# Kernel optimization log

Measured on AMD Instinct MI355X. Metric: run time of the kernel, lower is better.

Reference implementation:

```python
import jax, jax.numpy as jnp
import numpy as np
from jax.scipy.linalg import solve_triangular

B, S, H, D, L = 8, 256, 768, 128, 64


def setup_inputs() -> dict:
    key = jax.random.key(0)
    ks = jax.random.split(key, 14)
    f = lambda k, shp, s=1.0: (jax.random.normal(k, shp, dtype=jnp.float32) * s)
    return {
        'word_feat_mean': f(ks[0], (B, S, H)),
        'word_feat_div': f(ks[1], (B, S, H)),
        'sent_feat_mean': f(ks[2], (B, 1, H)),
        'sent_feat_div': f(ks[3], (B, 1, H)),
        'W1': f(ks[4], (H, D), 0.02), 'b1': f(ks[5], (D,), 0.02),
        'W2': f(ks[6], (H, D), 0.02), 'b2': f(ks[7], (D,), 0.02),
        'W3': f(ks[8], (H, D), 0.02), 'b3': f(ks[9], (D,), 0.02),
        'W4': f(ks[10], (H, D), 0.02), 'b4': f(ks[11], (D,), 0.02),
        'label_mean': f(ks[12], (L, D)),
        'label_div_vec': f(ks[13], (L, D)),
    }


def _jsd_rank1(mu_p, v_p, mu_q, v_q):
    """Symmetric Gaussian JSD (0.5*(KL12+KL21)) between N(mu_p, I+v_p v_p^T) (labels, [L,D])
    and N(mu_q, I+v_q v_q^T) (words, [B,S,D]) via Sherman-Morrison closed form -> [B,L,S].
    Same math as torch.distributions MVN KL with Sigma = I + vv^T."""
    d = mu_p.shape[-1]
    n_p = 1.0 + jnp.sum(v_p * v_p, -1)            # [L]   = det(I+vp vp^T)
    n_q = 1.0 + jnp.sum(v_q * v_q, -1)            # [B,S]
    dot = jnp.einsum('ld,bsd->bls', v_p, v_q)     # vp.vq
    # ||mu_q - mu_p||^2 expanded without materializing [B,L,S,D]
    d2 = (jnp.sum(mu_q * mu_q, -1)[:, None, :]
          - 2.0 * jnp.einsum('ld,bsd->bls', mu_p, mu_q)
          + jnp.sum(mu_p * mu_p, -1)[None, :, None])
    vq_delta = (jnp.einsum('bsd,bsd->bs', v_q, mu_q)[:, None, :]
                - jnp.einsum('ld,bsd->bls', mu_p, v_q))
    vp_delta = (jnp.einsum('ld,bsd->bls', v_p, mu_q)
                - jnp.sum(v_p * mu_p, -1)[None, :, None])
    n_p_b = n_p[None, :, None]
    n_q_b = n_q[:, None, :]
    maha_q = d2 - vq_delta ** 2 / n_q_b           # delta^T Sigma_q^{-1} delta
    maha_p = d2 - vp_delta ** 2 / n_p_b
    tr_pq = d + (n_p_b - 1.0) - ((n_q_b - 1.0) + dot ** 2) / n_q_b  # tr(Sq^{-1} Sp)
    tr_qp = d + (n_q_b - 1.0) - ((n_p_b - 1.0) + dot ** 2) / n_p_b
    kl_pq = 0.5 * (jnp.log(n_q_b) - jnp.log(n_p_b) - d + tr_pq + maha_q)
    kl_qp = 0.5 * (jnp.log(n_p_b) - jnp.log(n_q_b) - d + tr_qp + maha_p)
    return 0.5 * (kl_pq + kl_qp)


def _jsd_full(mu_p, S_p, mu_q, S_q):
    """Symmetric JSD between full-covariance Gaussians, Cholesky-based (like torch MVN KL).
    mu_*: [..., D], S_*: [..., D, D] -> [...]."""
    d = mu_p.shape[-1]
    L_p = jnp.linalg.cholesky(S_p)
    L_q = jnp.linalg.cholesky(S_q)
    logdet_p = 2.0 * jnp.sum(jnp.log(jnp.diagonal(L_p, axis1=-2, axis2=-1)), -1)
    logdet_q = 2.0 * jnp.sum(jnp.log(jnp.diagonal(L_q, axis1=-2, axis2=-1)), -1)
    delta = mu_q - mu_p

    def kl(La, Lb, logda, logdb):
        # KL(a||b) = 0.5*(logdet_b - logdet_a - d + tr(Sb^{-1}Sa) + delta^T Sb^{-1} delta)
        X = solve_triangular(Lb, La, lower=True)
        tr = jnp.sum(X * X, axis=(-1, -2))
        y = solve_triangular(Lb, delta[..., None], lower=True)[..., 0]
        maha = jnp.sum(y * y, -1)
        return 0.5 * (logdb - logda - d + tr + maha)

    return 0.5 * (kl(L_p, L_q, logdet_p, logdet_q) + kl(L_q, L_p, logdet_q, logdet_p))


def reference(word_feat_mean, word_feat_div, sent_feat_mean, sent_feat_div,
              W1, b1, W2, b2, W3, b3, W4, b4, label_mean, label_div_vec):
    Bx, Sx, _ = word_feat_mean.shape
    Dx = W1.shape[1]
    Lx = label_mean.shape[0]
    wm = word_feat_mean @ W1 + b1        # jw1: [B,S,D]
    wv = word_feat_div @ W2 + b2         # jw2: [B,S,D]
    sm = sent_feat_mean @ W3 + b3        # jw3: [B,1,D]
    sv = sent_feat_div @ W4 + b4         # jw4: [B,1,D]
    eye = jnp.eye(Dx, dtype=wm.dtype)
    # Gaussian JSD attention: q = labels, k = v = words (closed-form, no [B,L*S,D,D])
    score = jax.nn.softmax(_jsd_rank1(label_mean, label_div_vec, wm, wv), axis=-1)  # [B,L,S]
    v_mean = jnp.einsum('bls,bsd->bld', score, wm)
    word_cov = eye + wv[..., :, None] * wv[..., None, :]                 # [B,S,D,D]
    v_div = jnp.einsum('bls,bsde->blde', score, word_cov)                # [B,L,D,D]
    sent_cov = eye + sv[..., :, None] * sv[..., None, :]                 # [B,1,D,D]
    text_mean = (sm + v_mean) / 2                                        # [B,L,D]
    text_div = (sent_cov + v_div) / 2                                    # [B,L,D,D]
    label_cov = eye + label_div_vec[:, :, None] * label_div_vec[:, None, :]  # [L,D,D]
    lm_b = jnp.broadcast_to(label_mean, (Bx, Lx, Dx))
    lc_b = jnp.broadcast_to(label_cov, (Bx, Lx, Dx, Dx))
    relate_score = _jsd_full(text_mean, text_div, lm_b, lc_b)            # [B,L]
    return relate_score, lm_b, lc_b
```

## Files before the change

### kernel.cpp

```cpp
#include <hip/hip_runtime.h>
#include <hip/hip_bf16.h>


#define PITCH 132

typedef __attribute__((ext_vector_type(8))) short bf16x8;
typedef __attribute__((ext_vector_type(4))) float f32x4;

__device__ __forceinline__ float bf2f(unsigned int u) {
    union { unsigned int i; float f; } c; c.i = u << 16; return c.f;
}
__device__ __forceinline__ unsigned short f2bf(float f) {
    __hip_bfloat16 h = __float2bfloat16(f);
    union { __hip_bfloat16 h; unsigned short u; } c; c.h = h; return c.u;
}

__global__ __launch_bounds__(256, 2)
void k1_gemm(const float* __restrict__ Am, const float* __restrict__ Av,
             const float* __restrict__ sfm, const float* __restrict__ sfd,
             const float* __restrict__ W1, const float* __restrict__ B1,
             const float* __restrict__ W2, const float* __restrict__ B2,
             const float* __restrict__ W3, const float* __restrict__ B3,
             const float* __restrict__ W4, const float* __restrict__ B4,
             const float* __restrict__ lm, const float* __restrict__ ldv,
             float* __restrict__ wm, float* __restrict__ wv,
             float* __restrict__ sm, float* __restrict__ sv,
             float4* __restrict__ labscg,
             unsigned short* __restrict__ wvTg) {
    const int tid = threadIdx.x;
    const int sel = blockIdx.y;
    if (blockIdx.x == 257) {
        if (sel == 0) {
            int l = tid >> 2, q = tid & 3;
            const float* mr = lm + (size_t)l * 128 + q * 32;
            const float* vr = ldv + (size_t)l * 128 + q * 32;
            float s0 = 0.f, s1 = 0.f, s2 = 0.f;
            for (int k = 0; k < 32; k += 4) {
                float4 m = *(const float4*)&mr[k];
                float4 v = *(const float4*)&vr[k];
                s0 += m.x * m.x + m.y * m.y + m.z * m.z + m.w * m.w;
                s1 += v.x * v.x + v.y * v.y + v.z * v.z + v.w * v.w;
                s2 += m.x * v.x + m.y * v.y + m.z * v.z + m.w * v.w;
            }
            s0 += __shfl_xor(s0, 1); s0 += __shfl_xor(s0, 2);
            s1 += __shfl_xor(s1, 1); s1 += __shfl_xor(s1, 2);
            s2 += __shfl_xor(s2, 1); s2 += __shfl_xor(s2, 2);
            if (q == 0) labscg[l] = make_float4(s0, s1, s2, 0.f);
        }
        return;
    }
    __shared__ float At[8][64];
    __shared__ __align__(16) float Wt[64][128];
    __shared__ float tileT[8][129];
    const bool sentB = (blockIdx.x == 256);
    const float* A  = sentB ? (sel ? sfd : sfm) : (sel ? Av : Am);
    const float* W  = sentB ? (sel ? W4 : W3) : (sel ? W2 : W1);
    const float* Bs = sentB ? (sel ? B4 : B3) : (sel ? B2 : B1);
    float* D = sentB ? (sel ? sv : sm) : (sel ? wv : wm);
    const int R0 = sentB ? 0 : blockIdx.x * 8;
    const int r = tid >> 5;
    const int j0 = (tid & 31) * 4;
    float acc[4] = {0.f, 0.f, 0.f, 0.f};
    for (int k0 = 0; k0 < 768; k0 += 64) {
        __syncthreads();
        {
            int f = tid;
            At[f >> 6][f & 63] = A[(size_t)(R0 + (f >> 6)) * 768 + k0 + (f & 63)];
            f = tid + 256;
            At[f >> 6][f & 63] = A[(size_t)(R0 + (f >> 6)) * 768 + k0 + (f & 63)];
        }
#pragma unroll
        for (int it = 0; it < 8; ++it) {
            int f = tid + it * 256;
            int rr = f >> 5, c4 = (f & 31) * 4;
            *(float4*)&Wt[rr][c4] = *(const float4*)&W[(size_t)(k0 + rr) * 128 + c4];
        }
        __syncthreads();
#pragma unroll 16
        for (int kk = 0; kk < 64; ++kk) {
            float a = At[r][kk];
            float4 w0 = *(const float4*)&Wt[kk][j0];
            acc[0] += a * w0.x; acc[1] += a * w0.y; acc[2] += a * w0.z; acc[3] += a * w0.w;
        }
    }
    {
        float b0 = Bs[j0], b1 = Bs[j0 + 1], b2 = Bs[j0 + 2], b3 = Bs[j0 + 3];
        float4 o = make_float4(acc[0] + b0, acc[1] + b1, acc[2] + b2, acc[3] + b3);
        *(float4*)&D[(size_t)(R0 + r) * 128 + j0] = o;
        tileT[r][j0 + 0] = o.x; tileT[r][j0 + 1] = o.y;
        tileT[r][j0 + 2] = o.z; tileT[r][j0 + 3] = o.w;
    }
    if (sel && !sentB) {
        __syncthreads();
        if (tid < 128) {
            int d = tid;
            unsigned short u[8];
#pragma unroll
            for (int ss = 0; ss < 8; ++ss) u[ss] = f2bf(tileT[ss][d]);
            unsigned int p0 = (unsigned int)u[0] | ((unsigned int)u[1] << 16);
            unsigned int p1 = (unsigned int)u[2] | ((unsigned int)u[3] << 16);
            unsigned int p2 = (unsigned int)u[4] | ((unsigned int)u[5] << 16);
            unsigned int p3 = (unsigned int)u[6] | ((unsigned int)u[7] << 16);
            unsigned short* dst = wvTg + (size_t)(R0 >> 8) * 32768 + (size_t)d * 256 + (R0 & 255);
            *(uint4*)dst = make_uint4(p0, p1, p2, p3);
        }
    }
}

template <int N>
__device__ __forceinline__ void bsumN(float* v, float* red) {
#pragma unroll
    for (int o = 32; o; o >>= 1)
#pragma unroll
        for (int n = 0; n < N; ++n) v[n] += __shfl_xor(v[n], o);
    __syncthreads();
    if ((threadIdx.x & 63) == 0) {
        int w = threadIdx.x >> 6;
#pragma unroll
        for (int n = 0; n < N; ++n) red[w * N + n] = v[n];
    }
    __syncthreads();
#pragma unroll
    for (int n = 0; n < N; ++n)
        v[n] = red[0 * N + n] + red[1 * N + n] + red[2 * N + n] + red[3 * N + n];
    __syncthreads();
}

__global__ __launch_bounds__(256, 2)
void k4_fused(const float* __restrict__ wm, const float* __restrict__ wv,
              const unsigned short* __restrict__ wvTg,
              const float* __restrict__ smg, const float* __restrict__ svg,
              const float* __restrict__ lmg, const float* __restrict__ ldvg,
              const float4* __restrict__ labscg,
              float* __restrict__ out) {
    extern __shared__ float smem[];
    float* Amat = smem;
    float* Wb   = smem + 16896;
    float* ssq  = smem + 19008;
    float* svr  = smem + 19264;
    float* vrow = smem + 19392;
    float* zv   = smem + 19520;
    float* zd   = smem + 19648;
    float* red  = smem + 19776;
    float* scoreL = Amat;
    float* vpart  = Amat + 256;

    const int tid = threadIdx.x;
    const int bid = blockIdx.x;
    const int b = bid >> 6, l = bid & 63;

    if (tid < 128) {
        svr[tid]  = svg[b * 128 + tid];
        vrow[tid] = ldvg[l * 128 + tid];
        zv[tid]   = lmg[l * 128 + tid];
    }
    __syncthreads();
    if (tid < 32) {
        float4 v = *(const float4*)&lmg[l * 128 + tid * 4];
        *(float4*)&out[512 + (size_t)bid * 128 + tid * 4] = v;
    }
    {
        float* lcb = out + 512 + 65536 + (size_t)bid * 16384;
#pragma unroll
        for (int q = 0; q < 16; ++q) {
            int flat4 = q * 256 + tid;
            int i = flat4 >> 5;
            int j4 = (flat4 & 31) * 4;
            float vi = vrow[i];
            float4 r;
            r.x = vi * vrow[j4 + 0] + ((i == j4 + 0) ? 1.f : 0.f);
            r.y = vi * vrow[j4 + 1] + ((i == j4 + 1) ? 1.f : 0.f);
            r.z = vi * vrow[j4 + 2] + ((i == j4 + 2) ? 1.f : 0.f);
            r.w = vi * vrow[j4 + 3] + ((i == j4 + 3) ? 1.f : 0.f);
            *(float4*)&lcb[(size_t)flat4 * 4] = r;
        }
    }
    float4 lsv = labscg[l];
    const float mmp = lsv.x, np = 1.f + lsv.y, vmp = lsv.z;
    const float4* wmr = (const float4*)(wm + (size_t)(b * 256 + tid) * 128);
    const float4* wvr = (const float4*)(wv + (size_t)(b * 256 + tid) * 128);
    float md = 0.f, dot = 0.f, pvv = 0.f, vq = 0.f;
    float smm = 0.f, svv = 0.f, smv = 0.f;
#pragma unroll 8
    for (int q = 0; q < 32; ++q) {
        float4 xm = wmr[q], xv = wvr[q];
        const float* m4 = &zv[q * 4];
        const float* v4 = &vrow[q * 4];
        md  += m4[0] * xm.x + m4[1] * xm.y + m4[2] * xm.z + m4[3] * xm.w;
        dot += v4[0] * xv.x + v4[1] * xv.y + v4[2] * xv.z + v4[3] * xv.w;
        pvv += m4[0] * xv.x + m4[1] * xv.y + m4[2] * xv.z + m4[3] * xv.w;
        vq  += v4[0] * xm.x + v4[1] * xm.y + v4[2] * xm.z + v4[3] * xm.w;
        smm += xm.x * xm.x + xm.y * xm.y + xm.z * xm.z + xm.w * xm.w;
        svv += xv.x * xv.x + xv.y * xv.y + xv.z * xv.z + xv.w * xv.w;
        smv += xm.x * xv.x + xm.y * xv.y + xm.z * xv.z + xm.w * xv.w;
    }
    float nq = 1.f + svv;
    float d2 = smm - 2.f * md + mmp;
    float vqd = smv - pvv, vpd = vq - vmp;
    float inq = 1.f / nq, inp = 1.f / np;
    float maha_q = d2 - vqd * vqd * inq;
    float maha_p = d2 - vpd * vpd * inp;
    float logit = 0.25f * ((np - 1.f) + (nq - 1.f)
                           - (nq - 1.f + dot * dot) * inq
                           - (np - 1.f + dot * dot) * inp
                           + maha_q + maha_p);
    float mx = logit;
#pragma unroll
    for (int o = 32; o; o >>= 1) mx = fmaxf(mx, __shfl_xor(mx, o));
    if ((tid & 63) == 0) red[tid >> 6] = mx;
    __syncthreads();
    mx = fmaxf(fmaxf(red[0], red[1]), fmaxf(red[2], red[3]));
    float e = expf(logit - mx);
    float s = e;
#pragma unroll
    for (int o = 32; o; o >>= 1) s += __shfl_xor(s, o);
    __syncthreads();
    if ((tid & 63) == 0) red[tid >> 6] = s;
    __syncthreads();
    float tot = red[0] + red[1] + red[2] + red[3];
    float sc = e / tot;
    scoreL[tid] = sc;
    ssq[tid] = sqrtf(sc);
    __syncthreads();
    {
        int d4 = (tid & 31) * 4, sg = tid >> 5;
        const float* wmb = wm + (size_t)b * 256 * 128;
        float ax = 0.f, ay = 0.f, az = 0.f, aw = 0.f;
        for (int s2 = sg * 32; s2 < sg * 32 + 32; ++s2) {
            float w = scoreL[s2];
            float4 x = *(const float4*)&wmb[(size_t)s2 * 128 + d4];
            ax += w * x.x; ay += w * x.y; az += w * x.z; aw += w * x.w;
        }
        *(float4*)&vpart[sg * 128 + d4] = make_float4(ax, ay, az, aw);
    }
    __syncthreads();
    if (tid < 128) {
        float vm8 = 0.f;
#pragma unroll
        for (int g2 = 0; g2 < 8; ++g2) vm8 += vpart[g2 * 128 + tid];
        zd[tid] = zv[tid] - 0.5f * (smg[b * 128 + tid] + vm8);
        zv[tid] = vrow[tid];
    }
    __syncthreads();
    {
        unsigned short* Sb = (unsigned short*)Amat;
        const unsigned short* src = wvTg + (size_t)b * 32768;
        const int s0 = (tid & 31) * 8;
        float ssv[8];
#pragma unroll
        for (int j = 0; j < 8; ++j) ssv[j] = ssq[s0 + j];
#pragma unroll
        for (int it = 0; it < 16; ++it) {
            int f8 = tid + it * 256;
            int d = f8 >> 5;
            uint4 raw = *(const uint4*)&src[(size_t)f8 * 8];
            unsigned int p0 = (unsigned int)f2bf(bf2f(raw.x & 0xffffu) * ssv[0])
                            | ((unsigned int)f2bf(bf2f(raw.x >> 16) * ssv[1]) << 16);
            unsigned int p1 = (unsigned int)f2bf(bf2f(raw.y & 0xffffu) * ssv[2])
                            | ((unsigned int)f2bf(bf2f(raw.y >> 16) * ssv[3]) << 16);
            unsigned int p2 = (unsigned int)f2bf(bf2f(raw.z & 0xffffu) * ssv[4])
                            | ((unsigned int)f2bf(bf2f(raw.z >> 16) * ssv[5]) << 16);
            unsigned int p3 = (unsigned int)f2bf(bf2f(raw.w & 0xffffu) * ssv[6])
                            | ((unsigned int)f2bf(bf2f(raw.w >> 16) * ssv[7]) << 16);
            *(uint4*)&Sb[(size_t)d * 264 + s0] = make_uint4(p0, p1, p2, p3);
        }
    }
    __syncthreads();
    {
        const unsigned short* Sb = (const unsigned short*)Amat;
        const int w = tid >> 6, ln = tid & 63;
        const int rl = ln & 15, g = ln >> 4;
        const int arow0 = 16 * w + rl;
        const int arow1 = 16 * (w + 4) + rl;
        f32x4 acc0[8], acc1[8];
#pragma unroll
        for (int t = 0; t < 8; ++t) {
            acc0[t] = (f32x4){0.f, 0.f, 0.f, 0.f};
            acc1[t] = (f32x4){0.f, 0.f, 0.f, 0.f};
        }
#pragma unroll
        for (int ks = 0; ks < 8; ++ks) {
            bf16x8 a0 = *(const bf16x8*)&Sb[(size_t)arow0 * 264 + ks * 32 + g * 8];
            bf16x8 a1 = *(const bf16x8*)&Sb[(size_t)arow1 * 264 + ks * 32 + g * 8];
#pragma unroll
            for (int tj = 0; tj < 8; ++tj) {
                bf16x8 bb = *(const bf16x8*)&Sb[(size_t)(16 * tj + rl) * 264 + ks * 32 + g * 8];
                acc0[tj] = __builtin_amdgcn_mfma_f32_16x16x32_bf16(a0, bb, acc0[tj], 0, 0, 0);
                acc1[tj] = __builtin_amdgcn_mfma_f32_16x16x32_bf16(a1, bb, acc1[tj], 0, 0, 0);
            }
        }
        __syncthreads();
#pragma unroll
        for (int tj = 0; tj < 8; ++tj) {
            int j = 16 * tj + rl;
            float svj = svr[j];
#pragma unroll
            for (int r = 0; r < 4; ++r) {
                int i = 16 * w + g * 4 + r;
                Amat[i * PITCH + j] = ((i == j) ? 1.f : 0.f) + 0.5f * (svr[i] * svj + acc0[tj][r]);
                int i2 = 16 * (w + 4) + g * 4 + r;
                Amat[i2 * PITCH + j] = ((i2 == j) ? 1.f : 0.f) + 0.5f * (svr[i2] * svj + acc1[tj][r]);
            }
        }
    }
    __syncthreads();
    float v5[5] = {0.f, 0.f, 0.f, 0.f, 0.f};
    if (tid < 128) {
        v5[0] = Amat[tid * PITCH + tid];
        float vv = vrow[tid], de = zd[tid];
        v5[1] = vv * vv; v5[2] = de * de; v5[3] = vv * de;
    }
    {
        int i = tid >> 1, h = tid & 1;
        const float* Ar = &Amat[i * PITCH + h * 64];
        const float* vr = &vrow[h * 64];
        float s2 = 0.f;
        for (int k2 = 0; k2 < 64; k2 += 4) {
            float4 a = *(const float4*)&Ar[k2];
            s2 += a.x * vr[k2] + a.y * vr[k2 + 1] + a.z * vr[k2 + 2] + a.w * vr[k2 + 3];
        }
        v5[4] = vrow[i] * s2;
    }
    bsumN<5>(v5, red);
    const float trP = v5[0], nv = v5[1], dds = v5[2], vds = v5[3], vsv = v5[4];
    for (int p = 0; p < 8; ++p) {
        const int base = 16 * p;
        const int R = 112 - base;
        __syncthreads();
        if (p > 0) {
            const int pb = base - 16;
            if (tid >= base && tid < 128) {
                int i = tid;
                const float* Lr = &Amat[i * PITCH + pb];
                float dv = 0.f, dd2 = 0.f;
#pragma unroll
                for (int t = 0; t < 16; ++t) {
                    float lvv = Lr[t];
                    dv  += lvv * zv[pb + t];
                    dd2 += lvv * zd[pb + t];
                }
                zv[i] -= dv; zd[i] -= dd2;
            }
            int njobs = (R + 16) * 16;
            for (int idx = tid; idx < njobs; idx += 256) {
                int r2 = idx >> 4, jc = idx & 15;
                int i = base + r2, j = base + jc;
                if (j <= i) {
                    const float* wi = &Wb[i];
                    const float* wj = &Wb[j];
                    float acc2 = 0.f;
#pragma unroll
                    for (int t2 = 0; t2 < 16; ++t2)
                        acc2 += wi[t2 * PITCH] * wj[t2 * PITCH];
                    Amat[i * PITCH + j] -= acc2;
                }
            }
        }
        __syncthreads();
        if (tid < 64) {
            const int c = tid;
            float cv[16];
            if (c < 16) {
#pragma unroll
                for (int r2 = 0; r2 < 16; ++r2) {
                    int hi = (r2 >= c) ? r2 : c, lo2 = (r2 >= c) ? c : r2;
                    cv[r2] = Amat[(base + hi) * PITCH + base + lo2];
                }
            } else {
#pragma unroll
                for (int r2 = 0; r2 < 16; ++r2) cv[r2] = 0.f;
            }
#pragma unroll
            for (int t = 0; t < 16; ++t) {
                float lt[16];
#pragma unroll
                for (int r2 = 0; r2 < 16; ++r2) lt[r2] = __shfl(cv[r2], t);
                float invs = 1.f / sqrtf(lt[t]);
                if (c == t) {
#pragma unroll
                    for (int r2 = 0; r2 < 16; ++r2) cv[r2] = (r2 >= t) ? lt[r2] * invs : 0.f;
                } else if (c > t && c < 16) {
                    float lc = lt[c] * invs;
#pragma unroll
                    for (int r2 = 0; r2 < 16; ++r2)
                        if (r2 > t) cv[r2] -= (lt[r2] * invs) * lc;
                }
            }
            float x[16], acb[16];
#pragma unroll
            for (int r2 = 0; r2 < 16; ++r2) acb[r2] = 0.f;
#pragma unroll
            for (int r2 = 0; r2 < 16; ++r2) {
                float Lrr = __shfl(cv[r2], r2);
                float xr = (((c == r2) ? 1.f : 0.f) - acb[r2]) / Lrr;
                x[r2] = xr;
#pragma unroll
                for (int q = r2 + 1; q < 16; ++q) acb[q] += __shfl(cv[q], r2) * xr;
            }
            if (c < 16) {
#pragma unroll
                for (int r2 = 0; r2 < 16; ++r2)
                    Amat[(base + c) * PITCH + base + r2] = x[r2];
            }
            if (c < 32) {
                int t2 = c & 15;
                float* zp = (c < 16) ? zv : zd;
                float a0 = 0.f;
#pragma unroll
                for (int a = 0; a < 16; ++a)
                    a0 += Amat[(base + a) * PITCH + base + t2] * zp[base + a];
                zp[base + t2] = a0;
            }
        } else if (p > 0 && R > 0) {
            int nt = R >> 3;
            int ntri = (nt * (nt + 1)) >> 1;
            for (int tau = tid - 64; tau < ntri; tau += 192) {
                float ft = sqrtf(8.f * (float)tau + 1.f);
                int tr = (int)((ft - 1.f) * 0.5f);
                while (((tr + 1) * (tr + 2)) / 2 <= tau) ++tr;
                while ((tr * (tr + 1)) / 2 > tau) --tr;
                int tc = tau - ((tr * (tr + 1)) >> 1);
                int ii = base + 16 + tr * 8, jj = base + 16 + tc * 8;
                float a2[8][8];
#pragma unroll
                for (int r2 = 0; r2 < 8; ++r2)
#pragma unroll
                    for (int c2 = 0; c2 < 8; ++c2) a2[r2][c2] = 0.f;
#pragma unroll
                for (int t = 0; t < 16; ++t) {
                    const float* wr = &Wb[t * PITCH];
                    float4 x0 = *(const float4*)&wr[ii];
                    float4 x1 = *(const float4*)&wr[ii + 4];
                    float4 y0 = *(const float4*)&wr[jj];
                    float4 y1 = *(const float4*)&wr[jj + 4];
                    float xa[8] = {x0.x,x0.y,x0.z,x0.w, x1.x,x1.y,x1.z,x1.w};
                    float yb[8] = {y0.x,y0.y,y0.z,y0.w, y1.x,y1.y,y1.z,y1.w};
#pragma unroll
                    for (int r2 = 0; r2 < 8; ++r2)
#pragma unroll
                        for (int c2 = 0; c2 < 8; ++c2) a2[r2][c2] += xa[r2] * yb[c2];
                }
#pragma unroll
                for (int r2 = 0; r2 < 8; ++r2) {
                    float* Ar2 = &Amat[(ii + r2) * PITCH + jj];
                    float4 u0 = *(float4*)&Ar2[0];
                    float4 u1 = *(float4*)&Ar2[4];
                    u0.x -= a2[r2][0]; u0.y -= a2[r2][1]; u0.z -= a2[r2][2]; u0.w -= a2[r2][3];
                    u1.x -= a2[r2][4]; u1.y -= a2[r2][5]; u1.z -= a2[r2][6]; u1.w -= a2[r2][7];
                    *(float4*)&Ar2[0] = u0;
                    *(float4*)&Ar2[4] = u1;
                }
            }
        }
        __syncthreads();
        if (R > 0 && tid < R) {
            int i = base + 16 + tid;
            const float* Ar = &Amat[i * PITCH + base];
            float4 q0 = *(const float4*)&Ar[0];
            float4 q1 = *(const float4*)&Ar[4];
            float4 q2 = *(const float4*)&Ar[8];
            float4 q3 = *(const float4*)&Ar[12];
            float rA[16] = {q0.x,q0.y,q0.z,q0.w, q1.x,q1.y,q1.z,q1.w,
                            q2.x,q2.y,q2.z,q2.w, q3.x,q3.y,q3.z,q3.w};
            float lo[16];
#pragma unroll
            for (int t = 0; t < 16; ++t) lo[t] = 0.f;
#pragma unroll
            for (int a = 0; a < 16; ++a) {
                float va = rA[a];
                const float* Trow = &Amat[(base + a) * PITCH + base];
                float4 t0 = *(const float4*)&Trow[0];
                float4 t1 = *(const float4*)&Trow[4];
                float4 t2 = *(const float4*)&Trow[8];
                float4 t3 = *(const float4*)&Trow[12];
                lo[0] += va * t0.x; lo[1] += va * t0.y; lo[2] += va * t0.z; lo[3] += va * t0.w;
                lo[4] += va * t1.x; lo[5] += va * t1.y; lo[6] += va * t1.z; lo[7] += va * t1.w;
                lo[8] += va * t2.x; lo[9] += va * t2.y; lo[10] += va * t2.z; lo[11] += va * t2.w;
                lo[12] += va * t3.x; lo[13] += va * t3.y; lo[14] += va * t3.z; lo[15] += va * t3.w;
            }
            float* Aw = &Amat[i * PITCH + base];
            *(float4*)&Aw[0]  = make_float4(lo[0], lo[1], lo[2], lo[3]);
            *(float4*)&Aw[4]  = make_float4(lo[4], lo[5], lo[6], lo[7]);
            *(float4*)&Aw[8]  = make_float4(lo[8], lo[9], lo[10], lo[11]);
            *(float4*)&Aw[12] = make_float4(lo[12], lo[13], lo[14], lo[15]);
#pragma unroll
            for (int t = 0; t < 16; ++t) Wb[t * PITCH + i] = lo[t];
        }
    }
    __syncthreads();
    for (int t = tid; t < 128; t += 256) {
        int q = t >> 5, tt = t & 31;
        int c0 = (tt >> 2) * 2, r0 = (tt & 3) * 4;
        int rb = 32 * q + 16, cb = 32 * q;
        float a4[2][4] = {{0,0,0,0},{0,0,0,0}};
        for (int k = 0; k < 16; k += 4) {
            float4 xc0 = *(const float4*)&Amat[(cb + c0) * PITCH + cb + k];
            float4 xc1 = *(const float4*)&Amat[(cb + c0 + 1) * PITCH + cb + k];
#pragma unroll
            for (int rr = 0; rr < 4; ++rr) {
                float4 lr = *(const float4*)&Amat[(rb + r0 + rr) * PITCH + cb + k];
                a4[0][rr] += xc0.x * lr.x + xc0.y * lr.y + xc0.z * lr.z + xc0.w * lr.w;
                a4[1][rr] += xc1.x * lr.x + xc1.y * lr.y + xc1.z * lr.z + xc1.w * lr.w;
            }
        }
#pragma unroll
        for (int cc = 0; cc < 2; ++cc)
#pragma unroll
            for (int rr = 0; rr < 4; ++rr)
                Wb[q * 256 + (c0 + cc) * 16 + (r0 + rr)] = a4[cc][rr];
    }
    __syncthreads();
    for (int t = tid; t < 128; t += 256) {
        int q = t >> 5, tt = t & 31;
        int c0 = (tt >> 2) * 2, r0 = (tt & 3) * 4;
        int rb = 32 * q + 16, cb = 32 * q;
        float a4[2][4] = {{0,0,0,0},{0,0,0,0}};
        for (int a = 0; a < 16; ++a) {
            float y0 = Wb[q * 256 + c0 * 16 + a];
            float y1 = Wb[q * 256 + (c0 + 1) * 16 + a];
            float4 t2 = *(const float4*)&Amat[(rb + a) * PITCH + rb + r0];
            a4[0][0] += y0 * t2.x; a4[0][1] += y0 * t2.y; a4[0][2] += y0 * t2.z; a4[0][3] += y0 * t2.w;
            a4[1][0] += y1 * t2.x; a4[1][1] += y1 * t2.y; a4[1][2] += y1 * t2.z; a4[1][3] += y1 * t2.w;
        }
#pragma unroll
        for (int cc = 0; cc < 2; ++cc)
#pragma unroll
            for (int rr = 0; rr < 4; ++rr)
                Amat[(cb + c0 + cc) * PITCH + rb + r0 + rr] = -a4[cc][rr];
    }
    __syncthreads();
    {
        int q = tid >> 7, tt = tid & 127;
        int c0 = (tt >> 3) * 2, r0 = (tt & 7) * 4;
        int rb = 64 * q + 32, cb = 64 * q;
        int ks = c0 & ~15;
        float a4[2][4] = {{0,0,0,0},{0,0,0,0}};
        for (int k = ks; k < 32; k += 4) {
            float4 xc0 = *(const float4*)&Amat[(cb + c0) * PITCH + cb + k];
            float4 xc1 = *(const float4*)&Amat[(cb + c0 + 1) * PITCH + cb + k];
#pragma unroll
            for (int rr = 0; rr < 4; ++rr) {
                float4 lr = *(const float4*)&Amat[(rb + r0 + rr) * PITCH + cb + k];
                a4[0][rr] += xc0.x * lr.x + xc0.y * lr.y + xc0.z * lr.z + xc0.w * lr.w;
                a4[1][rr] += xc1.x * lr.x + xc1.y * lr.y + xc1.z * lr.z + xc1.w * lr.w;
            }
        }
#pragma unroll
        for (int cc = 0; cc < 2; ++cc)
#pragma unroll
            for (int rr = 0; rr < 4; ++rr)
                Wb[q * 1024 + (c0 + cc) * 32 + (r0 + rr)] = a4[cc][rr];
    }
    __syncthreads();
    {
        int q = tid >> 7, tt = tid & 127;
        int c0 = (tt >> 3) * 2, r0 = (tt & 7) * 4;
        int rb = 64 * q + 32, cb = 64 * q;
        int atop = (r0 & ~15) + 15;
        float a4[2][4] = {{0,0,0,0},{0,0,0,0}};
        for (int a = 0; a <= atop; ++a) {
            float y0 = Wb[q * 1024 + c0 * 32 + a];
            float y1 = Wb[q * 1024 + (c0 + 1) * 32 + a];
            float4 t2 = *(const float4*)&Amat[(rb + a) * PITCH + rb + r0];
            a4[0][0] += y0 * t2.x; a4[0][1] += y0 * t2.y; a4[0][2] += y0 * t2.z; a4[0][3] += y0 * t2.w;
            a4[1][0] += y1 * t2.x; a4[1][1] += y1 * t2.y; a4[1][2] += y1 * t2.z; a4[1][3] += y1 * t2.w;
        }
#pragma unroll
        for (int cc = 0; cc < 2; ++cc)
#pragma unroll
            for (int rr = 0; rr < 4; ++rr)
                Amat[(cb + c0 + cc) * PITCH + rb + r0 + rr] = -a4[cc][rr];
    }
    __syncthreads();
#pragma unroll
    for (int h3 = 0; h3 < 2; ++h3) {
        const int ch = 32 * h3;
        {
            int c0 = (tid >> 4) * 2, r0 = (tid & 15) * 4;
            int ks = (ch + c0) & ~15;
            float a4[2][4] = {{0,0,0,0},{0,0,0,0}};
            for (int k = ks; k < 64; k += 4) {
                float4 xc0 = *(const float4*)&Amat[(ch + c0) * PITCH + k];
                float4 xc1 = *(const float4*)&Amat[(ch + c0 + 1) * PITCH + k];
#pragma unroll
                for (int rr = 0; rr < 4; ++rr) {
                    float4 lr = *(const float4*)&Amat[(64 + r0 + rr) * PITCH + k];
                    a4[0][rr] += xc0.x * lr.x + xc0.y * lr.y + xc0.z * lr.z + xc0.w * lr.w;
                    a4[1][rr] += xc1.x * lr.x + xc1.y * lr.y + xc1.z * lr.z + xc1.w * lr.w;
                }
            }
#pragma unroll
            for (int cc = 0; cc < 2; ++cc)
#pragma unroll
                for (int rr = 0; rr < 4; ++rr)
                    Wb[(c0 + cc) * 64 + r0 + rr] = a4[cc][rr];
        }
        __syncthreads();
        {
            int c0 = (tid >> 4) * 2, r0 = (tid & 15) * 4;
            int atop = (r0 & ~15) + 15;
            float a4[2][4] = {{0,0,0,0},{0,0,0,0}};
            for (int a = 0; a <= atop; ++a) {
                float y0 = Wb[c0 * 64 + a];
                float y1 = Wb[(c0 + 1) * 64 + a];
                float4 t2 = *(const float4*)&Amat[(64 + a) * PITCH + 64 + r0];
                a4[0][0] += y0 * t2.x; a4[0][1] += y0 * t2.y; a4[0][2] += y0 * t2.z; a4[0][3] += y0 * t2.w;
                a4[1][0] += y1 * t2.x; a4[1][1] += y1 * t2.y; a4[1][2] += y1 * t2.z; a4[1][3] += y1 * t2.w;
            }
#pragma unroll
            for (int cc = 0; cc < 2; ++cc)
#pragma unroll
                for (int rr = 0; rr < 4; ++rr)
                    Amat[(ch + c0 + cc) * PITCH + 64 + r0 + rr] = -a4[cc][rr];
        }
        __syncthreads();
    }
    float v3[3] = {0.f, 0.f, 0.f};
    {
        int i = tid & 127, h = tid >> 7;
        int c0 = (i >> 4) << 4;
        int half = (128 - c0) >> 1;
        const float* Ar = &Amat[i * PITCH + c0 + h * half];
        for (int k2 = 0; k2 < half; k2 += 4) {
            float4 a = *(const float4*)&Ar[k2];
            v3[0] += a.x * a.x + a.y * a.y + a.z * a.z + a.w * a.w;
        }
    }
    if (tid < 128) {
        float a = zv[tid];  v3[1] = a * a;
        float d22 = zd[tid]; v3[2] = d22 * d22;
    }
    bsumN<3>(v3, red);
    if (tid == 0) {
        float n = 1.f + nv;
        float Aterm = trP - vsv / n;
        float Bt = v3[0] + v3[1];
        float mq = dds - vds * vds / n;
        out[bid] = 0.25f * (Aterm + Bt - 256.f + mq + v3[2]);
    }
}

extern "C" void kernel_launch(void* const* d_in, const int* in_sizes, int n_in,
                              void* d_out, int out_size, void* d_ws, size_t ws_size,
                              hipStream_t stream) {
    const float* wfm = (const float*)d_in[0];
    const float* wfd = (const float*)d_in[1];
    const float* sfm = (const float*)d_in[2];
    const float* sfd = (const float*)d_in[3];
    const float* W1 = (const float*)d_in[4];
    const float* B1 = (const float*)d_in[5];
    const float* W2 = (const float*)d_in[6];
    const float* B2 = (const float*)d_in[7];
    const float* W3 = (const float*)d_in[8];
    const float* B3 = (const float*)d_in[9];
    const float* W4 = (const float*)d_in[10];
    const float* B4 = (const float*)d_in[11];
    const float* lm = (const float*)d_in[12];
    const float* ldv = (const float*)d_in[13];
    float* out = (float*)d_out;
    float* ws = (float*)d_ws;

    float* wm = ws;
    float* wv = ws + 262144;
    float* sm = ws + 524288;
    float* sv = ws + 525312;
    float4* labscg = (float4*)(ws + 526336);
    unsigned short* wvTg = (unsigned short*)(ws + 731392);

    constexpr int SH_FLOATS = 19800;
    constexpr size_t SH_BYTES = SH_FLOATS * sizeof(float);
    (void)hipFuncSetAttribute((const void*)k4_fused,
                              hipFuncAttributeMaxDynamicSharedMemorySize,
                              (int)SH_BYTES);

    k1_gemm<<<dim3(258, 2), 256, 0, stream>>>(wfm, wfd, sfm, sfd,
                                              W1, B1, W2, B2, W3, B3, W4, B4,
                                              lm, ldv, wm, wv, sm, sv, labscg, wvTg);
    k4_fused<<<512, 256, SH_BYTES, stream>>>(wm, wv, wvTg, sm, sv, lm, ldv, labscg, out);
}
```

Measured before the change: 174.2 us.

## Fold deferred Cholesky updates into diagonal-block and trailing-update phases to cut barriers

Removes one of the per-panel barrier phases of the blocked Cholesky. The diagonal-block rank-16 update now runs in wave 0 via shuffles, and the panel and z-vector updates are done by the other waves alongside the trailing update. The z-vector triangular solve moves after the panel solve, running on otherwise idle threads. The softmax reduction uses separate scratch slots so one barrier can be dropped. Correctness now depends on the reordered data dependencies still holding: the z solve reads the inverted diagonal block and the panel reads the updated entries.

```diff
diff --git a/kernel.cpp b/kernel.cpp
--- a/kernel.cpp
+++ b/kernel.cpp
@@ -214,10 +214,9 @@
     float s = e;
 #pragma unroll
     for (int o = 32; o; o >>= 1) s += __shfl_xor(s, o);
-    __syncthreads();
-    if ((tid & 63) == 0) red[tid >> 6] = s;
-    __syncthreads();
-    float tot = red[0] + red[1] + red[2] + red[3];
+    if ((tid & 63) == 0) red[8 + (tid >> 6)] = s;
+    __syncthreads();
+    float tot = red[8] + red[9] + red[10] + red[11];
     float sc = e / tot;
     scoreL[tid] = sc;
     ssq[tid] = sqrtf(sc);
@@ -327,36 +326,6 @@
         const int base = 16 * p;
         const int R = 112 - base;
         __syncthreads();
-        if (p > 0) {
-            const int pb = base - 16;
-            if (tid >= base && tid < 128) {
-                int i = tid;
-                const float* Lr = &Amat[i * PITCH + pb];
-                float dv = 0.f, dd2 = 0.f;
-#pragma unroll
-                for (int t = 0; t < 16; ++t) {
-                    float lvv = Lr[t];
-                    dv  += lvv * zv[pb + t];
-                    dd2 += lvv * zd[pb + t];
-                }
-                zv[i] -= dv; zd[i] -= dd2;
-            }
-            int njobs = (R + 16) * 16;
-            for (int idx = tid; idx < njobs; idx += 256) {
-                int r2 = idx >> 4, jc = idx & 15;
-                int i = base + r2, j = base + jc;
-                if (j <= i) {
-                    const float* wi = &Wb[i];
-                    const float* wj = &Wb[j];
-                    float acc2 = 0.f;
-#pragma unroll
-                    for (int t2 = 0; t2 < 16; ++t2)
-                        acc2 += wi[t2 * PITCH] * wj[t2 * PITCH];
-                    Amat[i * PITCH + j] -= acc2;
-                }
-            }
-        }
-        __syncthreads();
         if (tid < 64) {
             const int c = tid;
             float cv[16];
@@ -366,6 +335,19 @@
                     int hi = (r2 >= c) ? r2 : c, lo2 = (r2 >= c) ? c : r2;
                     cv[r2] = Amat[(base + hi) * PITCH + base + lo2];
                 }
+                if (p > 0) {
+                    float wbc[16];
+#pragma unroll
+                    for (int t = 0; t < 16; ++t) wbc[t] = Wb[t * PITCH + base + c];
+#pragma unroll
+                    for (int r2 = 0; r2 < 16; ++r2) {
+                        float acc2 = 0.f;
+#pragma unroll
+                        for (int t = 0; t < 16; ++t)
+                            acc2 += __shfl(wbc[t], r2) * wbc[t];
+                        cv[r2] -= acc2;
+                    }
+                }
             } else {
 #pragma unroll
                 for (int r2 = 0; r2 < 16; ++r2) cv[r2] = 0.f;
@@ -402,53 +384,71 @@
                 for (int r2 = 0; r2 < 16; ++r2)
                     Amat[(base + c) * PITCH + base + r2] = x[r2];
             }
-            if (c < 32) {
-                int t2 = c & 15;
-                float* zp = (c < 16) ? zv : zd;
-                float a0 = 0.f;
-#pragma unroll
-                for (int a = 0; a < 16; ++a)
-                    a0 += Amat[(base + a) * PITCH + base + t2] * zp[base + a];
-                zp[base + t2] = a0;
-            }
-        } else if (p > 0 && R > 0) {
-            int nt = R >> 3;
-            int ntri = (nt * (nt + 1)) >> 1;
-            for (int tau = tid - 64; tau < ntri; tau += 192) {
-                float ft = sqrtf(8.f * (float)tau + 1.f);
-                int tr = (int)((ft - 1.f) * 0.5f);
-                while (((tr + 1) * (tr + 2)) / 2 <= tau) ++tr;
-                while ((tr * (tr + 1)) / 2 > tau) --tr;
-                int tc = tau - ((tr * (tr + 1)) >> 1);
-                int ii = base + 16 + tr * 8, jj = base + 16 + tc * 8;
-                float a2[8][8];
-#pragma unroll
-                for (int r2 = 0; r2 < 8; ++r2)
-#pragma unroll
-                    for (int c2 = 0; c2 < 8; ++c2) a2[r2][c2] = 0.f;
-#pragma unroll
-                for (int t = 0; t < 16; ++t) {
-                    const float* wr = &Wb[t * PITCH];
-                    float4 x0 = *(const float4*)&wr[ii];
-                    float4 x1 = *(const float4*)&wr[ii + 4];
-                    float4 y0 = *(const float4*)&wr[jj];
-                    float4 y1 = *(const float4*)&wr[jj + 4];
-                    float xa[8] = {x0.x,x0.y,x0.z,x0.w, x1.x,x1.y,x1.z,x1.w};
-                    float yb[8] = {y0.x,y0.y,y0.z,y0.w, y1.x,y1.y,y1.z,y1.w};
+        } else if (p > 0) {
+            const int pb = base - 16;
+            int t = tid - 64;
+            if (t < 128 - base) {
+                int i = base + t;
+                const float* Lr = &Amat[i * PITCH + pb];
+                float dv = 0.f, dd2 = 0.f;
+#pragma unroll
+                for (int t2 = 0; t2 < 16; ++t2) {
+                    float lvv = Lr[t2];
+                    dv  += lvv * zv[pb + t2];
+                    dd2 += lvv * zd[pb + t2];
+                }
+                zv[i] -= dv; zd[i] -= dd2;
+            }
+            for (int idx = t; idx < R * 16; idx += 192) {
+                int r2 = idx >> 4, jc = idx & 15;
+                int i = base + 16 + r2, j = base + jc;
+                const float* wi = &Wb[i];
+                const float* wj = &Wb[j];
+                float acc2 = 0.f;
+#pragma unroll
+                for (int t2 = 0; t2 < 16; ++t2)
+                    acc2 += wi[t2 * PITCH] * wj[t2 * PITCH];
+                Amat[i * PITCH + j] -= acc2;
+            }
+            if (R > 0) {
+                int nt = R >> 3;
+                int ntri = (nt * (nt + 1)) >> 1;
+                for (int tau = t; tau < ntri; tau += 192) {
+                    float ft = sqrtf(8.f * (float)tau + 1.f);
+                    int tr = (int)((ft - 1.f) * 0.5f);
+                    while (((tr + 1) * (tr + 2)) / 2 <= tau) ++tr;
+                    while ((tr * (tr + 1)) / 2 > tau) --tr;
+                    int tc = tau - ((tr * (tr + 1)) >> 1);
+                    int ii = base + 16 + tr * 8, jj = base + 16 + tc * 8;
+                    float a2[8][8];
 #pragma unroll
                     for (int r2 = 0; r2 < 8; ++r2)
 #pragma unroll
-                        for (int c2 = 0; c2 < 8; ++c2) a2[r2][c2] += xa[r2] * yb[c2];
-                }
-#pragma unroll
-                for (int r2 = 0; r2 < 8; ++r2) {
-                    float* Ar2 = &Amat[(ii + r2) * PITCH + jj];
-                    float4 u0 = *(float4*)&Ar2[0];
-                    float4 u1 = *(float4*)&Ar2[4];
-                    u0.x -= a2[r2][0]; u0.y -= a2[r2][1]; u0.z -= a2[r2][2]; u0.w -= a2[r2][3];
-                    u1.x -= a2[r2][4]; u1.y -= a2[r2][5]; u1.z -= a2[r2][6]; u1.w -= a2[r2][7];
-                    *(float4*)&Ar2[0] = u0;
-                    *(float4*)&Ar2[4] = u1;
+                        for (int c2 = 0; c2 < 8; ++c2) a2[r2][c2] = 0.f;
+#pragma unroll
+                    for (int t2 = 0; t2 < 16; ++t2) {
+                        const float* wr = &Wb[t2 * PITCH];
+                        float4 x0 = *(const float4*)&wr[ii];
+                        float4 x1 = *(const float4*)&wr[ii + 4];
+                        float4 y0 = *(const float4*)&wr[jj];
+                        float4 y1 = *(const float4*)&wr[jj + 4];
+                        float xa[8] = {x0.x,x0.y,x0.z,x0.w, x1.x,x1.y,x1.z,x1.w};
+                        float yb[8] = {y0.x,y0.y,y0.z,y0.w, y1.x,y1.y,y1.z,y1.w};
+#pragma unroll
+                        for (int r2 = 0; r2 < 8; ++r2)
+#pragma unroll
+                            for (int c2 = 0; c2 < 8; ++c2) a2[r2][c2] += xa[r2] * yb[c2];
+                    }
+#pragma unroll
+                    for (int r2 = 0; r2 < 8; ++r2) {
+                        float* Ar2 = &Amat[(ii + r2) * PITCH + jj];
+                        float4 u0 = *(float4*)&Ar2[0];
+                        float4 u1 = *(float4*)&Ar2[4];
+                        u0.x -= a2[r2][0]; u0.y -= a2[r2][1]; u0.z -= a2[r2][2]; u0.w -= a2[r2][3];
+                        u1.x -= a2[r2][4]; u1.y -= a2[r2][5]; u1.z -= a2[r2][6]; u1.w -= a2[r2][7];
+                        *(float4*)&Ar2[0] = u0;
+                        *(float4*)&Ar2[4] = u1;
+                    }
                 }
             }
         }
@@ -485,6 +485,15 @@
             *(float4*)&Aw[12] = make_float4(lo[12], lo[13], lo[14], lo[15]);
 #pragma unroll
             for (int t = 0; t < 16; ++t) Wb[t * PITCH + i] = lo[t];
+        }
+        if (tid >= 128 && tid < 160) {
+            int t2 = (tid - 128) & 15;
+            float* zp = (tid < 144) ? zv : zd;
+            float a0 = 0.f;
+#pragma unroll
+            for (int a = 0; a < 16; ++a)
+                a0 += Amat[(base + a) * PITCH + base + t2] * zp[base + a];
+            zp[base + t2] = a0;
         }
     }
     __syncthreads();
```

Measured after the change: 173.5 us, median of 3. About the same (-0.4%).
